# Performance work log

Hardware: AMD Instinct MI355X
Metric: run time of the kernel (lower is better)

## Reference

```python
import jax, jax.numpy as jnp
import numpy as np
from jax import lax

WIN_SIZE = 11
SIGMA = 1.5
CHANNELS = 3
C1 = (0.01 * 255) ** 2
C2 = (0.03 * 255) ** 2


def fspecial_gauss(size, sigma, channels):
    x, y = np.mgrid[-size // 2 + 1:size // 2 + 1, -size // 2 + 1:size // 2 + 1]
    g = np.exp(-((x ** 2 + y ** 2) / (2.0 * sigma ** 2)))
    g = (g / g.sum()).astype(np.float32)
    # depthwise kernel, OIHW with I=1, O=channels
    return jnp.asarray(np.tile(g[None, None], (channels, 1, 1, 1)))


def _gauss_filter(x, win):
    # depthwise valid conv, NCHW
    return lax.conv_general_dilated(
        x, win, window_strides=(1, 1), padding='VALID',
        feature_group_count=x.shape[1],
        dimension_numbers=('NCHW', 'OIHW', 'NCHW'))


def setup_inputs() -> dict:
    key = jax.random.key(0)
    k1, k2 = jax.random.split(key)
    X = jax.random.uniform(k1, (32, 3, 512, 512), dtype=jnp.float32)
    Y = jax.random.uniform(k2, (32, 3, 512, 512), dtype=jnp.float32)
    win = fspecial_gauss(WIN_SIZE, SIGMA, CHANNELS)
    return {"X": X, "Y": Y, "win": win}


def reference(X, Y, win):
    mu1 = _gauss_filter(X, win)
    mu2 = _gauss_filter(Y, win)
    mu1_sq = mu1 * mu1
    mu2_sq = mu2 * mu2
    mu1_mu2 = mu1 * mu2
    sigma1_sq = _gauss_filter(X * X, win) - mu1_sq
    sigma2_sq = _gauss_filter(Y * Y, win) - mu2_sq
    sigma12 = _gauss_filter(X * Y, win) - mu1_mu2
    cs_map = jax.nn.relu((2 * sigma12 + C2) / (sigma1_sq + sigma2_sq + C2))
    ssim_map = (2 * mu1_mu2 + C1) / (mu1_sq + mu2_sq + C1) * cs_map
    ssim_val = jnp.mean(ssim_map, axis=(1, 2, 3))  # per-image SSIM
    return 1.0 - jnp.mean(ssim_val)  # as_loss=True
```

## Files before the change

### kernel.cpp

```cpp
#include <hip/hip_runtime.h>
#include <math.h>


#define WIN   11
#define IMG   512
#define OUT_N 502
#define TO_R  32
#define TO_C  64
#define TI_C  (TO_C + WIN - 1)
#define VB_W  77
#define C1F   6.5025f
#define C2F   58.5225f

struct GaussW { float w[WIN]; };

__global__ __launch_bounds__(256) void ssim_v5_kernel(
    const float* __restrict__ X, const float* __restrict__ Y,
    GaussW gw, double* __restrict__ acc)
{
    __shared__ float vb[5][TO_R][VB_W];

    const int plane = blockIdx.z;
    const int ox0 = blockIdx.x * TO_C;
    const int oy0 = blockIdx.y * TO_R;
    const float* Xp = X + (size_t)plane * IMG * IMG;
    const float* Yp = Y + (size_t)plane * IMG * IMG;
    const int tid  = threadIdx.x;
    const int wave = tid >> 6;
    const int lane = tid & 63;

    {
        const int s  = wave;
        const int r0 = oy0 + s * 8;
        for (int c = lane; c < TI_C; c += 64) {
            int gc = ox0 + c; if (gc > IMG - 1) gc = IMG - 1;

            float a0[8] = {0}, a1[8] = {0}, a2[8] = {0}, a3[8] = {0}, a4[8] = {0};
#pragma unroll
            for (int k = 0; k < 18; ++k) {
                int gr = r0 + k; if (gr > IMG - 1) gr = IMG - 1;
                size_t off = (size_t)gr * IMG + gc;
                float x = Xp[off];
                float y = Yp[off];
                float xx = x * x, yy = y * y, xy = x * y;
                const int jlo = (k > 10) ? (k - 10) : 0;
                const int jhi = (k < 7) ? k : 7;
#pragma unroll
                for (int j = jlo; j <= jhi; ++j) {
                    float wv = gw.w[k - j];
                    a0[j] += wv * x;
                    a1[j] += wv * y;
                    a2[j] += wv * xx;
                    a3[j] += wv * yy;
                    a4[j] += wv * xy;
                }
            }
#pragma unroll
            for (int j = 0; j < 8; ++j) {
                int i = s * 8 + j;
                vb[0][i][c] = a0[j];
                vb[1][i][c] = a1[j];
                vb[2][i][c] = a2[j];
                vb[3][i][c] = a3[j];
                vb[4][i][c] = a4[j];
            }
        }
    }
    __syncthreads();

    const int i  = tid >> 3;
    const int c0 = (tid & 7) * 8;
    const int gi = oy0 + i;
    float m[5][8];
#pragma unroll
    for (int f = 0; f < 5; ++f) {
        float v[18];
#pragma unroll
        for (int k = 0; k < 18; ++k) v[k] = vb[f][i][c0 + k];
#pragma unroll
        for (int oc = 0; oc < 8; ++oc) {
            float s = 0.f;
#pragma unroll
            for (int k = 0; k < WIN; ++k) s += gw.w[k] * v[oc + k];
            m[f][oc] = s;
        }
    }

    float psum = 0.f;
#pragma unroll
    for (int oc = 0; oc < 8; ++oc) {
        int gj = ox0 + c0 + oc;
        if (gi < OUT_N && gj < OUT_N) {
            float m1 = m[0][oc], m2 = m[1][oc];
            float mu1s = m1 * m1, mu2s = m2 * m2, mu12 = m1 * m2;
            float sig1  = m[2][oc] - mu1s;
            float sig2  = m[3][oc] - mu2s;
            float sig12 = m[4][oc] - mu12;
            float num = (2.f * mu12 + C1F) * (2.f * sig12 + C2F);
            float den = (mu1s + mu2s + C1F) * (sig1 + sig2 + C2F);
            num = fmaxf(num, 0.f);
            psum += num * __builtin_amdgcn_rcpf(den);
        }
    }

#pragma unroll
    for (int off = 32; off > 0; off >>= 1)
        psum += __shfl_down(psum, off, 64);
    __shared__ float wsum[4];
    if ((tid & 63) == 0) wsum[tid >> 6] = psum;
    __syncthreads();
    if (tid == 0) {
        float s = wsum[0] + wsum[1] + wsum[2] + wsum[3];
        atomicAdd(acc, (double)s);
    }
}

__global__ void ssim_finalize_kernel(const double* __restrict__ acc,
                                     float* __restrict__ out)
{
    if (threadIdx.x == 0 && blockIdx.x == 0) {
        const double count = (double)96 * OUT_N * OUT_N;
        out[0] = (float)(1.0 - (*acc) / count);
    }
}

extern "C" void kernel_launch(void* const* d_in, const int* in_sizes, int n_in,
                              void* d_out, int out_size, void* d_ws, size_t ws_size,
                              hipStream_t stream) {
    (void)in_sizes; (void)n_in; (void)out_size; (void)ws_size;
    const float* X = (const float*)d_in[0];
    const float* Y = (const float*)d_in[1];
    float* out = (float*)d_out;
    double* acc = (double*)d_ws;

    hipMemsetAsync(d_ws, 0, sizeof(double), stream);

    GaussW gw;
    {
        double g[WIN], s = 0.0;
        for (int i = 0; i < WIN; ++i) {
            double d = (double)(i - 5);
            g[i] = exp(-(d * d) / (2.0 * 1.5 * 1.5));
            s += g[i];
        }
        for (int i = 0; i < WIN; ++i) gw.w[i] = (float)(g[i] / s);
    }

    dim3 grid((OUT_N + TO_C - 1) / TO_C,
              (OUT_N + TO_R - 1) / TO_R,
              96);
    ssim_v5_kernel<<<grid, 256, 0, stream>>>(X, Y, gw, acc);
    ssim_finalize_kernel<<<1, 64, 0, stream>>>(acc, out);
}
```

Before: 314.3 us.

## Specialize vertical pass by boundary, split tail columns, fuse finalize via last-block

Restructures the vertical-filter stage so each lane does exactly one column task. Row clamping is compiled in only for the bottom row of blocks, and column clamping only for the 10 halo columns, which wave 0 handles separately. The separate finalize kernel is removed: the last block, found with an atomic counter and threadfences, writes the loss. This removes the strided column loop's uneven second iteration and one kernel launch, but wave 0 now does extra serial work for the halo columns, which may create imbalance within the block.

Measured after the change: 570.5 us. +81.5%, slower.

```diff
diff --git a/kernel.cpp b/kernel.cpp
--- a/kernel.cpp
+++ b/kernel.cpp
@@ -11,12 +11,56 @@
 #define VB_W  77
 #define C1F   6.5025f
 #define C2F   58.5225f
+#define GRID_X 8
+#define GRID_Y 16
+#define GRID_Z 96
+#define NBLOCKS (GRID_X * GRID_Y * GRID_Z)
 
 struct GaussW { float w[WIN]; };
 
-__global__ __launch_bounds__(256) void ssim_v5_kernel(
+template<bool CR, bool CC>
+__device__ __forceinline__ void vert_task(
+    const float* __restrict__ Xp, const float* __restrict__ Yp,
+    const GaussW& gw, float (*vb)[TO_R][VB_W],
+    int r0, int gc, int i0, int c)
+{
+    if (CC) gc = min(gc, IMG - 1);
+    float a0[8] = {0}, a1[8] = {0}, a2[8] = {0}, a3[8] = {0}, a4[8] = {0};
+#pragma unroll
+    for (int k = 0; k < 18; ++k) {
+        int gr = r0 + k;
+        if (CR) gr = min(gr, IMG - 1);
+        size_t off = (size_t)gr * IMG + gc;
+        float x = Xp[off];
+        float y = Yp[off];
+        float xx = x * x, yy = y * y, xy = x * y;
+        const int jlo = (k > 10) ? (k - 10) : 0;
+        const int jhi = (k < 7) ? k : 7;
+#pragma unroll
+        for (int j = jlo; j <= jhi; ++j) {
+            float wv = gw.w[k - j];
+            a0[j] += wv * x;
+            a1[j] += wv * y;
+            a2[j] += wv * xx;
+            a3[j] += wv * yy;
+            a4[j] += wv * xy;
+        }
+    }
+#pragma unroll
+    for (int j = 0; j < 8; ++j) {
+        int i = i0 + j;
+        vb[0][i][c] = a0[j];
+        vb[1][i][c] = a1[j];
+        vb[2][i][c] = a2[j];
+        vb[3][i][c] = a3[j];
+        vb[4][i][c] = a4[j];
+    }
+}
+
+__global__ __launch_bounds__(256) void ssim_v6_kernel(
     const float* __restrict__ X, const float* __restrict__ Y,
-    GaussW gw, double* __restrict__ acc)
+    GaussW gw, double* __restrict__ acc, unsigned int* __restrict__ done,
+    float* __restrict__ out)
 {
     __shared__ float vb[5][TO_R][VB_W];
 
@@ -30,41 +74,17 @@
     const int lane = tid & 63;
 
     {
-        const int s  = wave;
-        const int r0 = oy0 + s * 8;
-        for (int c = lane; c < TI_C; c += 64) {
-            int gc = ox0 + c; if (gc > IMG - 1) gc = IMG - 1;
-
-            float a0[8] = {0}, a1[8] = {0}, a2[8] = {0}, a3[8] = {0}, a4[8] = {0};
-#pragma unroll
-            for (int k = 0; k < 18; ++k) {
-                int gr = r0 + k; if (gr > IMG - 1) gr = IMG - 1;
-                size_t off = (size_t)gr * IMG + gc;
-                float x = Xp[off];
-                float y = Yp[off];
-                float xx = x * x, yy = y * y, xy = x * y;
-                const int jlo = (k > 10) ? (k - 10) : 0;
-                const int jhi = (k < 7) ? k : 7;
-#pragma unroll
-                for (int j = jlo; j <= jhi; ++j) {
-                    float wv = gw.w[k - j];
-                    a0[j] += wv * x;
-                    a1[j] += wv * y;
-                    a2[j] += wv * xx;
-                    a3[j] += wv * yy;
-                    a4[j] += wv * xy;
-                }
-            }
-#pragma unroll
-            for (int j = 0; j < 8; ++j) {
-                int i = s * 8 + j;
-                vb[0][i][c] = a0[j];
-                vb[1][i][c] = a1[j];
-                vb[2][i][c] = a2[j];
-                vb[3][i][c] = a3[j];
-                vb[4][i][c] = a4[j];
-            }
-        }
+        const int r0 = __builtin_amdgcn_readfirstlane(oy0 + wave * 8);
+        const int gc = ox0 + lane;
+        if (blockIdx.y == GRID_Y - 1)
+            vert_task<true,  false>(Xp, Yp, gw, vb, r0, gc, wave * 8, lane);
+        else
+            vert_task<false, false>(Xp, Yp, gw, vb, r0, gc, wave * 8, lane);
+    }
+    if (wave == 0 && lane < 40) {
+        const int s = lane / 10;
+        const int c = TO_C + (lane - s * 10);
+        vert_task<true, true>(Xp, Yp, gw, vb, oy0 + s * 8, ox0 + c, s * 8, c);
     }
     __syncthreads();
 
@@ -112,15 +132,14 @@
     if (tid == 0) {
         float s = wsum[0] + wsum[1] + wsum[2] + wsum[3];
         atomicAdd(acc, (double)s);
-    }
-}
-
-__global__ void ssim_finalize_kernel(const double* __restrict__ acc,
-                                     float* __restrict__ out)
-{
-    if (threadIdx.x == 0 && blockIdx.x == 0) {
-        const double count = (double)96 * OUT_N * OUT_N;
-        out[0] = (float)(1.0 - (*acc) / count);
+        __threadfence();
+        unsigned prev = atomicAdd(done, 1u);
+        if (prev == NBLOCKS - 1) {
+            __threadfence();
+            double a = atomicAdd(acc, 0.0);
+            const double count = (double)GRID_Z * OUT_N * OUT_N;
+            out[0] = (float)(1.0 - a / count);
+        }
     }
 }
 
@@ -132,8 +151,9 @@
     const float* Y = (const float*)d_in[1];
     float* out = (float*)d_out;
     double* acc = (double*)d_ws;
+    unsigned int* done = (unsigned int*)((char*)d_ws + sizeof(double));
 
-    hipMemsetAsync(d_ws, 0, sizeof(double), stream);
+    hipMemsetAsync(d_ws, 0, 16, stream);
 
     GaussW gw;
     {
@@ -146,9 +166,6 @@
         for (int i = 0; i < WIN; ++i) gw.w[i] = (float)(g[i] / s);
     }
 
-    dim3 grid((OUT_N + TO_C - 1) / TO_C,
-              (OUT_N + TO_R - 1) / TO_R,
-              96);
-    ssim_v5_kernel<<<grid, 256, 0, stream>>>(X, Y, gw, acc);
-    ssim_finalize_kernel<<<1, 64, 0, stream>>>(acc, out);
+    dim3 grid(GRID_X, GRID_Y, GRID_Z);
+    ssim_v6_kernel<<<grid, 256, 0, stream>>>(X, Y, gw, acc, done, out);
 }
```
